# Performance work log

Hardware: AMD Instinct MI355X
Metric: run time of the kernel (lower is better)

## Reference

```python
import jax, jax.numpy as jnp
import numpy as np

N_HEAD = 16
HEAD_DIM = 128  # n_embd // n_head
RMS_EPS = 1.1920929e-07  # torch.finfo(float32).eps, F.rms_norm default
ROPE_BASE = 10000.0


def _rope_tables(T, head_dim, dtype=jnp.float32):
    half = head_dim // 2
    inv_freq = 1.0 / (ROPE_BASE ** (jnp.arange(half, dtype=jnp.float32) / half))
    t = jnp.arange(T, dtype=jnp.float32)
    freqs = jnp.outer(t, inv_freq)  # [T, half]
    return jnp.cos(freqs).astype(dtype), jnp.sin(freqs).astype(dtype)


def _apply_rope(x, cos, sin):
    # x: [B, T, H, D]; cos/sin: [T, D//2]
    half = x.shape[-1] // 2
    x1, x2 = x[..., :half], x[..., half:]
    c = cos[None, :, None, :]
    s = sin[None, :, None, :]
    return jnp.concatenate([x1 * c - x2 * s, x1 * s + x2 * c], axis=-1)


def _rms_norm(x):
    ms = jnp.mean(jnp.square(x), axis=-1, keepdims=True)
    return x * jax.lax.rsqrt(ms + RMS_EPS)


def setup_inputs() -> dict:
    key = jax.random.key(0)
    ks = jax.random.split(key, 5)
    B, T, E = 4, 2048, 2048
    x = jax.random.normal(ks[0], (B, T, E), dtype=jnp.float32)
    scale = 0.02
    wq = jax.random.normal(ks[1], (E, E), dtype=jnp.float32) * scale
    wk = jax.random.normal(ks[2], (E, E), dtype=jnp.float32) * scale
    wv = jax.random.normal(ks[3], (E, E), dtype=jnp.float32) * scale
    wo = jax.random.normal(ks[4], (E, E), dtype=jnp.float32) * scale
    return {"x": x, "wq": wq, "wk": wk, "wv": wv, "wo": wo}


def reference(x, wq, wk, wv, wo):
    B, T, E = x.shape
    H, D = N_HEAD, HEAD_DIM
    # QKV projections (bias-free linears)
    q = (x @ wq).reshape(B, T, H, D)
    k = (x @ wk).reshape(B, T, H, D)
    v = (x @ wv).reshape(B, T, H, D)
    # RoPE then parameter-free QK RMS norm
    cos, sin = _rope_tables(T, D, x.dtype)
    q = _rms_norm(_apply_rope(q, cos, sin))
    k = _rms_norm(_apply_rope(k, cos, sin))
    # causal SDPA
    scale = 1.0 / jnp.sqrt(jnp.asarray(D, dtype=x.dtype))
    scores = jnp.einsum('bqhd,bkhd->bhqk', q, k) * scale
    causal = jnp.tril(jnp.ones((T, T), dtype=bool))
    scores = jnp.where(causal[None, None], scores, jnp.asarray(-jnp.inf, scores.dtype))
    attn = jax.nn.softmax(scores, axis=-1)
    y = jnp.einsum('bhqk,bkhd->bqhd', attn, v).reshape(B, T, E)
    return y @ wo
```

## Files before the change

kernel.cpp:

```cpp
#include <hip/hip_runtime.h>
#include <math.h>

#define T_SEQ 2048
#define BATCH 4
#define E_DIM 2048
#define NHEAD 16
#define HDIM 128
#define RMS_EPS 1.1920929e-07f
#define NQT (T_SEQ / 128)

typedef unsigned short u16;
typedef __attribute__((ext_vector_type(8))) unsigned short u16x8;
typedef __attribute__((ext_vector_type(8))) short bf16x8;
typedef __attribute__((ext_vector_type(4))) float f32x4;

typedef const __attribute__((address_space(1))) unsigned int g_u32;
typedef __attribute__((address_space(3))) unsigned int l_u32;

static __device__ __forceinline__ u16 f2b(float f) {
  unsigned int u = __builtin_bit_cast(unsigned int, f);
  u += 0x7fffu + ((u >> 16) & 1u);
  return (u16)(u >> 16);
}
static __device__ __forceinline__ float b2f(u16 v) {
  return __builtin_bit_cast(float, ((unsigned int)v) << 16);
}

__global__ __launch_bounds__(256) void convert_f32_bf16(
    const float* __restrict__ src, u16* __restrict__ dst, int n) {
  int i = (blockIdx.x * 256 + threadIdx.x) * 4;
  if (i >= n) return;
  float4 v = *reinterpret_cast<const float4*>(src + i);
  ushort4 o;
  o.x = f2b(v.x); o.y = f2b(v.y); o.z = f2b(v.z); o.w = f2b(v.w);
  *reinterpret_cast<ushort4*>(dst + i) = o;
}

__global__ __launch_bounds__(256) void convt_w_k(
    const float* __restrict__ W, u16* __restrict__ Wt) {
  __shared__ u16 tile[64][72];
  int c0 = blockIdx.x * 64;
  int r0 = blockIdx.y * 64;
  int tid = threadIdx.x;
  int lrow = tid >> 2;
  int lcol = (tid & 3) * 16;
#pragma unroll
  for (int i = 0; i < 4; ++i) {
    float4 v = *reinterpret_cast<const float4*>(
        W + (long long)(r0 + lrow) * E_DIM + c0 + lcol + i * 4);
    tile[lrow][lcol + i * 4 + 0] = f2b(v.x);
    tile[lrow][lcol + i * 4 + 1] = f2b(v.y);
    tile[lrow][lcol + i * 4 + 2] = f2b(v.z);
    tile[lrow][lcol + i * 4 + 3] = f2b(v.w);
  }
  __syncthreads();
  int wrow = tid >> 2;
  int wcol = (tid & 3) * 16;
  u16 o[16];
#pragma unroll
  for (int i = 0; i < 16; ++i) o[i] = tile[wcol + i][wrow];
  u16* dst = Wt + (long long)(c0 + wrow) * E_DIM + r0 + wcol;
  *reinterpret_cast<u16x8*>(dst)     = *reinterpret_cast<u16x8*>(&o[0]);
  *reinterpret_cast<u16x8*>(dst + 8) = *reinterpret_cast<u16x8*>(&o[8]);
}

__global__ __launch_bounds__(256) void rope_tables_k(
    float* __restrict__ cost, float* __restrict__ sint) {
  int idx = blockIdx.x * 256 + threadIdx.x;
  int i = idx & 63, t = idx >> 6;
  double inv = pow(10000.0, -(double)i / 64.0);
  double ang = (double)t * inv;
  cost[idx] = (float)cos(ang);
  sint[idx] = (float)sin(ang);
}

__global__ __launch_bounds__(256) void rope_rms_k(
    u16* __restrict__ Qb, u16* __restrict__ Kb, const float* __restrict__ cost,
    const float* __restrict__ sint) {
  int half = gridDim.x >> 1;
  int isK = blockIdx.x >= half;
  u16* qk = isK ? Kb : Qb;
  float outscale = isK ? 1.0f : 0.08838834764831845f;
  int wave = threadIdx.x >> 6;
  int lane = threadIdx.x & 63;
  long long row = (long long)(blockIdx.x - (isK ? half : 0)) * 4 + wave;
  int th = (int)(row >> 4);
  int t = th & (T_SEQ - 1);
  u16* p = qk + row * HDIM;
  float x1 = b2f(p[lane]);
  float x2 = b2f(p[lane + 64]);
  float c = cost[t * 64 + lane];
  float s = sint[t * 64 + lane];
  float o1 = x1 * c - x2 * s;
  float o2 = x1 * s + x2 * c;
  float ss = o1 * o1 + o2 * o2;
#pragma unroll
  for (int m = 32; m >= 1; m >>= 1) ss += __shfl_xor(ss, m, 64);
  float r = rsqrtf(ss * (1.0f / 128.0f) + RMS_EPS) * outscale;
  p[lane] = f2b(o1 * r);
  p[lane + 64] = f2b(o2 * r);
}

__global__ __launch_bounds__(256) void transpose_v_k(
    const u16* __restrict__ V, u16* __restrict__ Vt) {
  __shared__ u16 tile[64][72];
  int t0 = blockIdx.x * 64, d0 = blockIdx.y * 64;
  int bh = blockIdx.z;
  int b = bh >> 4, h = bh & 15;
  int tid = threadIdx.x;
  int lrow = tid >> 3;
  int lcol = (tid & 7) * 8;
#pragma unroll
  for (int pass = 0; pass < 2; ++pass) {
    int row = lrow + pass * 32;
    const u16* src = V + ((((long long)b * T_SEQ + t0 + row) * NHEAD + h) << 7) + d0 + lcol;
    *reinterpret_cast<u16x8*>(&tile[row][lcol]) = *reinterpret_cast<const u16x8*>(src);
  }
  __syncthreads();
#pragma unroll
  for (int pass = 0; pass < 2; ++pass) {
    int drow = (tid >> 3) + pass * 32;
    int tcol = (tid & 7) * 8;
    u16x8 o;
#pragma unroll
    for (int i = 0; i < 8; ++i) o[i] = tile[tcol + i][drow];
    u16* dst = Vt + ((long long)bh * HDIM + d0 + drow) * T_SEQ + t0 + tcol;
    *reinterpret_cast<u16x8*>(dst) = o;
  }
}

__global__ __launch_bounds__(512, 2) void gemm_bt_k(
    const u16* __restrict__ A,
    const u16* __restrict__ Bt0, const u16* __restrict__ Bt1, const u16* __restrict__ Bt2,
    u16* __restrict__ C0, u16* __restrict__ C1, u16* __restrict__ C2,
    float* __restrict__ Cf, int M, int N, int K) {
  const u16* Bt = blockIdx.z == 0 ? Bt0 : (blockIdx.z == 1 ? Bt1 : Bt2);
  u16* C = blockIdx.z == 0 ? C0 : (blockIdx.z == 1 ? C1 : C2);
  __shared__ u16 As[2][256 * 64];
  __shared__ u16 Bs[2][256 * 64];
  const int tid = threadIdx.x;
  const int lane = tid & 63, wave = tid >> 6;
  const int wm = wave >> 2, wn = wave & 3;
  const int m0 = blockIdx.y * 256, n0 = blockIdx.x * 256;
  const int lr = lane & 15, lq = lane >> 4, l7 = lane & 7;
  const int NT = K >> 6;

  int rowA[2][2], rowB[2][2];
  const u16* gA[2][2];
  const u16* gB[2][2];
#pragma unroll
  for (int l = 0; l < 2; ++l) {
    int rihb = l * 64 + wave * 8;
#pragma unroll
    for (int h = 0; h < 2; ++h) {
      int ra = ((rihb >> 6) << 7) + h * 64 + (rihb & 63);
      int rb = ((rihb >> 5) << 6) + h * 32 + (rihb & 31);
      rowA[h][l] = ra;
      rowB[h][l] = rb;
      int rA = ra + (lane >> 3);
      int rB = rb + (lane >> 3);
      gA[h][l] = A + (long long)(m0 + rA) * K + ((l7 ^ (rA & 7)) * 8);
      gB[h][l] = Bt + (long long)(n0 + rB) * K + ((l7 ^ (rB & 7)) * 8);
    }
  }

  f32x4 acc[8][4] = {};

#define STAGE_A(tile, h)                                                      \
  do {                                                                        \
    if ((tile) < NT) {                                                        \
      int _b = (tile) & 1;                                                    \
      long long _ko = (long long)(tile) << 6;                                 \
      __builtin_amdgcn_global_load_lds((g_u32*)(gA[h][0] + _ko),              \
          (l_u32*)(&As[_b][rowA[h][0] * 64]), 16, 0, 0);                      \
      __builtin_amdgcn_global_load_lds((g_u32*)(gA[h][1] + _ko),              \
          (l_u32*)(&As[_b][rowA[h][1] * 64]), 16, 0, 0);                      \
    }                                                                         \
  } while (0)
#define STAGE_B(tile, h)                                                      \
  do {                                                                        \
    if ((tile) < NT) {                                                        \
      int _b = (tile) & 1;                                                    \
      long long _ko = (long long)(tile) << 6;                                 \
      __builtin_amdgcn_global_load_lds((g_u32*)(gB[h][0] + _ko),              \
          (l_u32*)(&Bs[_b][rowB[h][0] * 64]), 16, 0, 0);                      \
      __builtin_amdgcn_global_load_lds((g_u32*)(gB[h][1] + _ko),              \
          (l_u32*)(&Bs[_b][rowB[h][1] * 64]), 16, 0, 0);                      \
    }                                                                         \
  } while (0)

  STAGE_B(0, 0); STAGE_B(0, 1); STAGE_A(0, 0); STAGE_A(0, 1);
  STAGE_B(1, 0); STAGE_B(1, 1); STAGE_A(1, 0);
  asm volatile("s_waitcnt vmcnt(6)" ::: "memory");
  __builtin_amdgcn_s_barrier();
  __builtin_amdgcn_sched_barrier(0);

  for (int t = 0; t < NT; ++t) {
    const u16* Ab = As[t & 1];
    const u16* Bb = Bs[t & 1];
    bf16x8 aA[4][2], bB[4][2];

#define LD_A(mt, ks)                                                          \
  (*reinterpret_cast<const bf16x8*>(                                          \
      Ab + (wm * 128 + (mt) * 16 + lr) * 64 + ((((ks) << 2) + lq) ^ l7) * 8))
#define LD_B(nt, ks)                                                          \
  (*reinterpret_cast<const bf16x8*>(                                          \
      Bb + (wn * 64 + (nt) * 16 + lr) * 64 + ((((ks) << 2) + lq) ^ l7) * 8))
#define MFMA_QUAD(mh, nh)                                                     \
  _Pragma("unroll") for (int mi = 0; mi < 4; ++mi)                            \
  _Pragma("unroll") for (int ni = 0; ni < 2; ++ni)                            \
  _Pragma("unroll") for (int ks = 0; ks < 2; ++ks)                            \
    acc[(mh) * 4 + mi][(nh) * 2 + ni] =                                       \
        __builtin_amdgcn_mfma_f32_16x16x32_bf16(aA[mi][ks],                   \
            bB[(nh) * 2 + ni][ks], acc[(mh) * 4 + mi][(nh) * 2 + ni], 0, 0, 0);

#pragma unroll
    for (int mi = 0; mi < 4; ++mi) { aA[mi][0] = LD_A(mi, 0); aA[mi][1] = LD_A(mi, 1); }
#pragma unroll
    for (int ni = 0; ni < 2; ++ni) { bB[ni][0] = LD_B(ni, 0); bB[ni][1] = LD_B(ni, 1); }
    STAGE_A(t + 1, 1);
    __builtin_amdgcn_s_barrier();
    asm volatile("s_waitcnt lgkmcnt(0)" ::: "memory");
    __builtin_amdgcn_sched_barrier(0);
    __builtin_amdgcn_s_setprio(1);
    MFMA_QUAD(0, 0);
    __builtin_amdgcn_s_setprio(0);
    __builtin_amdgcn_s_barrier();

#pragma unroll
    for (int ni = 0; ni < 2; ++ni) { bB[2 + ni][0] = LD_B(2 + ni, 0); bB[2 + ni][1] = LD_B(2 + ni, 1); }
    STAGE_B(t + 2, 0);
    __builtin_amdgcn_s_barrier();
    asm volatile("s_waitcnt lgkmcnt(0)" ::: "memory");
    __builtin_amdgcn_sched_barrier(0);
    __builtin_amdgcn_s_setprio(1);
    MFMA_QUAD(0, 1);
    __builtin_amdgcn_s_setprio(0);
    __builtin_amdgcn_s_barrier();

#pragma unroll
    for (int mi = 0; mi < 4; ++mi) { aA[mi][0] = LD_A(4 + mi, 0); aA[mi][1] = LD_A(4 + mi, 1); }
    STAGE_B(t + 2, 1);
    __builtin_amdgcn_s_barrier();
    asm volatile("s_waitcnt lgkmcnt(0)" ::: "memory");
    __builtin_amdgcn_sched_barrier(0);
    __builtin_amdgcn_s_setprio(1);
    MFMA_QUAD(1, 0);
    __builtin_amdgcn_s_setprio(0);
    __builtin_amdgcn_s_barrier();

    STAGE_A(t + 2, 0);
    __builtin_amdgcn_s_barrier();
    __builtin_amdgcn_s_setprio(1);
    MFMA_QUAD(1, 1);
    __builtin_amdgcn_s_setprio(0);
    if (t < NT - 2) {
      asm volatile("s_waitcnt vmcnt(6)" ::: "memory");
    } else {
      asm volatile("s_waitcnt vmcnt(0)" ::: "memory");
    }
    __builtin_amdgcn_s_barrier();
    __builtin_amdgcn_sched_barrier(0);
  }
#undef LD_A
#undef LD_B
#undef MFMA_QUAD
#undef STAGE_A
#undef STAGE_B

#pragma unroll
  for (int mt = 0; mt < 8; ++mt)
#pragma unroll
    for (int nt = 0; nt < 4; ++nt) {
      long long col = n0 + wn * 64 + nt * 16 + lr;
#pragma unroll
      for (int r = 0; r < 4; ++r) {
        long long row = m0 + wm * 128 + mt * 16 + lq * 4 + r;
        float v = acc[mt][nt][r];
        if (Cf) Cf[row * N + col] = v;
        else C[row * N + col] = f2b(v);
      }
    }
}

__global__ __launch_bounds__(256, 3) void attn_k(
    const u16* __restrict__ Q, const u16* __restrict__ K,
    const u16* __restrict__ Vt, u16* __restrict__ Y) {
  __shared__ u16 Ks[64 * 128];
  __shared__ u16 Vs[128 * 64];
  __shared__ u16 Ps[4][32 * 72];
  __shared__ float Al[4][32];
  int pair = blockIdx.x;
  int bh = blockIdx.y;
  int b = bh >> 4, h = bh & 15;
  int tid = threadIdx.x, lane = tid & 63, wave = tid >> 6;
  int lr = lane & 15, lq = lane >> 4;

  const u16* kp[4];
  const u16* vp[4];
#pragma unroll
  for (int p = 0; p < 4; ++p) {
    int c = p * 256 + wave * 64 + lane;
    int key = c >> 4, sk = c & 15, gk = (sk - key) & 15;
    kp[p] = K + (((long long)b * T_SEQ + key) * NHEAD + h) * HDIM + gk * 8;
    int d = c >> 3, sv = c & 7, gv = (sv - d) & 7;
    vp[p] = Vt + ((long long)bh * HDIM + d) * T_SEQ + gv * 8;
  }

#pragma unroll 1
  for (int phase = 0; phase < 2; ++phase) {
    int qt = phase == 0 ? (NQT - 1 - pair) : pair;
    int qbase = qt * 128 + wave * 32;

    bf16x8 aq[2][4];
#pragma unroll
    for (int n2 = 0; n2 < 2; ++n2) {
      const u16* qp = Q + (((long long)b * T_SEQ + qbase + n2 * 16 + lr) * NHEAD + h) * HDIM;
#pragma unroll
      for (int kt = 0; kt < 4; ++kt)
        aq[n2][kt] = *reinterpret_cast<const bf16x8*>(qp + kt * 32 + lq * 8);
    }

    float m_s[2], l_s[2];
#pragma unroll
    for (int n2 = 0; n2 < 2; ++n2) { m_s[n2] = -INFINITY; l_s[n2] = 0.f; }
    f32x4 o[2][8] = {};

    int niter = 2 * qt + 2;
    for (int j = 0; j < niter; ++j) {
      __syncthreads();
#pragma unroll
      for (int p = 0; p < 4; ++p) {
        __builtin_amdgcn_global_load_lds(
            (g_u32*)(kp[p] + (long long)j * 64 * NHEAD * HDIM),
            (l_u32*)(Ks + p * 2048 + wave * 512), 16, 0, 0);
        __builtin_amdgcn_global_load_lds(
            (g_u32*)(vp[p] + j * 64),
            (l_u32*)(Vs + p * 2048 + wave * 512), 16, 0, 0);
      }
      __syncthreads();

      f32x4 s[4][2];
#pragma unroll
      for (int mt = 0; mt < 4; ++mt) {
        int key = mt * 16 + lr;
        bf16x8 ak[4];
#pragma unroll
        for (int kt = 0; kt < 4; ++kt) {
          int slot = (kt * 4 + lq + key) & 15;
          ak[kt] = *reinterpret_cast<const bf16x8*>(&Ks[key * 128 + slot * 8]);
        }
#pragma unroll
        for (int n2 = 0; n2 < 2; ++n2) {
          f32x4 acc = {};
#pragma unroll
          for (int kt = 0; kt < 4; ++kt)
            acc = __builtin_amdgcn_mfma_f32_16x16x32_bf16(ak[kt], aq[n2][kt], acc, 0, 0, 0);
          s[mt][n2] = acc;
        }
      }

      if (j >= 2 * qt) {
#pragma unroll
        for (int mt = 0; mt < 4; ++mt)
#pragma unroll
          for (int n2 = 0; n2 < 2; ++n2) {
            int q = qbase + n2 * 16 + lr;
#pragma unroll
            for (int r = 0; r < 4; ++r) {
              int key = j * 64 + mt * 16 + lq * 4 + r;
              if (key > q) s[mt][n2][r] = -INFINITY;
            }
          }
      }

      float alpha[2];
#pragma unroll
      for (int n2 = 0; n2 < 2; ++n2) {
        float mx = s[0][n2][0];
#pragma unroll
        for (int mt = 0; mt < 4; ++mt)
#pragma unroll
          for (int r = 0; r < 4; ++r) mx = fmaxf(mx, s[mt][n2][r]);
        mx = fmaxf(mx, __shfl_xor(mx, 16, 64));
        mx = fmaxf(mx, __shfl_xor(mx, 32, 64));
        float mn = fmaxf(m_s[n2], mx);
        alpha[n2] = __expf(m_s[n2] - mn);
        m_s[n2] = mn;
        float sum = 0.f;
        int q = n2 * 16 + lr;
#pragma unroll
        for (int mt = 0; mt < 4; ++mt) {
          ushort4 pk;
          float p0 = __expf(s[mt][n2][0] - mn);
          float p1 = __expf(s[mt][n2][1] - mn);
          float p2 = __expf(s[mt][n2][2] - mn);
          float p3 = __expf(s[mt][n2][3] - mn);
          sum += (p0 + p1) + (p2 + p3);
          pk.x = f2b(p0); pk.y = f2b(p1); pk.z = f2b(p2); pk.w = f2b(p3);
          *reinterpret_cast<ushort4*>(&Ps[wave][q * 72 + mt * 16 + lq * 4]) = pk;
        }
        sum += __shfl_xor(sum, 16, 64);
        sum += __shfl_xor(sum, 32, 64);
        l_s[n2] = l_s[n2] * alpha[n2] + sum;
      }

      if (lq == 0) {
        Al[wave][lr] = alpha[0];
        Al[wave][16 + lr] = alpha[1];
      }
#pragma unroll
      for (int q2 = 0; q2 < 2; ++q2) {
        f32x4 av = *reinterpret_cast<const f32x4*>(&Al[wave][q2 * 16 + lq * 4]);
#pragma unroll
        for (int r = 0; r < 4; ++r)
#pragma unroll
          for (int dt = 0; dt < 8; ++dt) o[q2][dt][r] *= av[r];
      }

#pragma unroll
      for (int kh = 0; kh < 2; ++kh) {
        bf16x8 ap[2];
#pragma unroll
        for (int q2 = 0; q2 < 2; ++q2)
          ap[q2] = *reinterpret_cast<const bf16x8*>(
              &Ps[wave][(q2 * 16 + lr) * 72 + kh * 32 + lq * 8]);
#pragma unroll
        for (int dt = 0; dt < 8; ++dt) {
          int d = dt * 16 + lr;
          int slot = (kh * 4 + lq + d) & 7;
          bf16x8 bv = *reinterpret_cast<const bf16x8*>(&Vs[d * 64 + slot * 8]);
#pragma unroll
          for (int q2 = 0; q2 < 2; ++q2)
            o[q2][dt] = __builtin_amdgcn_mfma_f32_16x16x32_bf16(ap[q2], bv, o[q2][dt], 0, 0, 0);
        }
      }
    }

    if (lq == 0) {
      Al[wave][lr] = l_s[0];
      Al[wave][16 + lr] = l_s[1];
    }
#pragma unroll
    for (int q2 = 0; q2 < 2; ++q2) {
      f32x4 lv = *reinterpret_cast<const f32x4*>(&Al[wave][q2 * 16 + lq * 4]);
#pragma unroll
      for (int r = 0; r < 4; ++r) {
        float inv = 1.0f / lv[r];
        int q = qbase + q2 * 16 + lq * 4 + r;
        u16* yp = Y + (((long long)b * T_SEQ + q) * NHEAD + h) * HDIM;
#pragma unroll
        for (int dt = 0; dt < 8; ++dt)
          yp[dt * 16 + lr] = f2b(o[q2][dt][r] * inv);
      }
    }
  }
}

extern "C" void kernel_launch(void* const* d_in, const int* in_sizes, int n_in,
                              void* d_out, int out_size, void* d_ws, size_t ws_size,
                              hipStream_t stream) {
  (void)in_sizes; (void)n_in; (void)out_size; (void)ws_size;
  const float* x  = (const float*)d_in[0];
  const float* wq = (const float*)d_in[1];
  const float* wk = (const float*)d_in[2];
  const float* wv = (const float*)d_in[3];
  const float* wo = (const float*)d_in[4];
  float* out = (float*)d_out;

  char* ws = (char*)d_ws;
  size_t off = 0;
  auto alloc = [&](size_t bytes) {
    char* p = ws + off;
    off += (bytes + 255) & ~(size_t)255;
    return p;
  };
  const size_t NTOK = (size_t)BATCH * T_SEQ;
  const size_t XE = NTOK * E_DIM;
  const size_t WE = (size_t)E_DIM * E_DIM;

  u16* xb  = (u16*)alloc(XE * 2);
  u16* wqt = (u16*)alloc(WE * 2);
  u16* wkt = (u16*)alloc(WE * 2);
  u16* wvt = (u16*)alloc(WE * 2);
  u16* wot = (u16*)alloc(WE * 2);
  u16* Qb  = (u16*)alloc(XE * 2);
  u16* Kb  = (u16*)alloc(XE * 2);
  u16* Vb  = (u16*)alloc(XE * 2);
  u16* Vt  = (u16*)alloc(XE * 2);
  u16* Yb  = (u16*)alloc(XE * 2);
  float* cost = (float*)alloc((size_t)T_SEQ * 64 * 4);
  float* sint = (float*)alloc((size_t)T_SEQ * 64 * 4);

  convert_f32_bf16<<<XE / 1024, 256, 0, stream>>>(x, xb, (int)XE);
  dim3 gw(E_DIM / 64, E_DIM / 64);
  convt_w_k<<<gw, 256, 0, stream>>>(wq, wqt);
  convt_w_k<<<gw, 256, 0, stream>>>(wk, wkt);
  convt_w_k<<<gw, 256, 0, stream>>>(wv, wvt);
  convt_w_k<<<gw, 256, 0, stream>>>(wo, wot);
  rope_tables_k<<<(T_SEQ * 64) / 256, 256, 0, stream>>>(cost, sint);

  dim3 gq(E_DIM / 256, NTOK / 256, 3);
  gemm_bt_k<<<gq, 512, 0, stream>>>(xb, wqt, wkt, wvt, Qb, Kb, Vb, nullptr,
                                    (int)NTOK, E_DIM, E_DIM);

  rope_rms_k<<<(unsigned)(NTOK * NHEAD / 4) * 2, 256, 0, stream>>>(Qb, Kb, cost, sint);

  dim3 gt(T_SEQ / 64, HDIM / 64, BATCH * NHEAD);
  transpose_v_k<<<gt, 256, 0, stream>>>(Vb, Vt);

  dim3 ga(NQT / 2, BATCH * NHEAD);
  attn_k<<<ga, 256, 0, stream>>>(Qb, Kb, Vt, Yb);

  dim3 go(E_DIM / 256, NTOK / 256, 1);
  gemm_bt_k<<<go, 512, 0, stream>>>(Yb, wot, wot, wot, nullptr, nullptr, nullptr, out,
                                    (int)NTOK, E_DIM, E_DIM);
}
```

Baseline: 685.8 us.

## Remap GEMM and attention block indices for locality and restructure GEMM MFMA phases

Remaps GEMM workgroup indices so that consecutive blocks, which the hardware distributes round-robin across XCDs, share A/B tiles within each XCD's L2. The same swizzle is applied to attention so heads land in XCD-local groups. The GEMM main loop now works on 2 M-subtiles by 4 N-subtiles per phase, which cuts A-fragment registers, and advances global pointers incrementally instead of recomputing offsets. The mapping hardcodes grid shapes, so other launch dimensions would compute wrong tiles.

```diff
diff --git a/kernel.cpp b/kernel.cpp
--- a/kernel.cpp
+++ b/kernel.cpp
@@ -134,14 +134,26 @@
     const u16* __restrict__ Bt0, const u16* __restrict__ Bt1, const u16* __restrict__ Bt2,
     u16* __restrict__ C0, u16* __restrict__ C1, u16* __restrict__ C2,
     float* __restrict__ Cf, int M, int N, int K) {
-  const u16* Bt = blockIdx.z == 0 ? Bt0 : (blockIdx.z == 1 ? Bt1 : Bt2);
-  u16* C = blockIdx.z == 0 ? C0 : (blockIdx.z == 1 ? C1 : C2);
+  int lin = blockIdx.x + (blockIdx.y << 3) + (blockIdx.z << 8);
+  int kx = lin & 7, ii = lin >> 3;
+  int by = ((kx >> 1) << 3) + (ii & 7);
+  int bx, bz;
+  if (gridDim.z == 3) {
+    int u = (kx & 1) * 12 + (ii >> 3);
+    bx = u & 7; bz = u >> 3;
+  } else {
+    bx = ((kx & 1) << 2) + (ii >> 3);
+    bz = 0;
+  }
+  const u16* Bt = bz == 0 ? Bt0 : (bz == 1 ? Bt1 : Bt2);
+  u16* C = bz == 0 ? C0 : (bz == 1 ? C1 : C2);
+
   __shared__ u16 As[2][256 * 64];
   __shared__ u16 Bs[2][256 * 64];
   const int tid = threadIdx.x;
   const int lane = tid & 63, wave = tid >> 6;
   const int wm = wave >> 2, wn = wave & 3;
-  const int m0 = blockIdx.y * 256, n0 = blockIdx.x * 256;
+  const int m0 = by * 256, n0 = bx * 256;
   const int lr = lane & 15, lq = lane >> 4, l7 = lane & 7;
   const int NT = K >> 6;
 
@@ -166,93 +178,97 @@
 
   f32x4 acc[8][4] = {};
 
-#define STAGE_A(tile, h)                                                      \
-  do {                                                                        \
-    if ((tile) < NT) {                                                        \
-      int _b = (tile) & 1;                                                    \
-      long long _ko = (long long)(tile) << 6;                                 \
-      __builtin_amdgcn_global_load_lds((g_u32*)(gA[h][0] + _ko),              \
-          (l_u32*)(&As[_b][rowA[h][0] * 64]), 16, 0, 0);                      \
-      __builtin_amdgcn_global_load_lds((g_u32*)(gA[h][1] + _ko),              \
-          (l_u32*)(&As[_b][rowA[h][1] * 64]), 16, 0, 0);                      \
-    }                                                                         \
-  } while (0)
-#define STAGE_B(tile, h)                                                      \
-  do {                                                                        \
-    if ((tile) < NT) {                                                        \
-      int _b = (tile) & 1;                                                    \
-      long long _ko = (long long)(tile) << 6;                                 \
-      __builtin_amdgcn_global_load_lds((g_u32*)(gB[h][0] + _ko),              \
-          (l_u32*)(&Bs[_b][rowB[h][0] * 64]), 16, 0, 0);                      \
-      __builtin_amdgcn_global_load_lds((g_u32*)(gB[h][1] + _ko),              \
-          (l_u32*)(&Bs[_b][rowB[h][1] * 64]), 16, 0, 0);                      \
-    }                                                                         \
-  } while (0)
-
-  STAGE_B(0, 0); STAGE_B(0, 1); STAGE_A(0, 0); STAGE_A(0, 1);
-  STAGE_B(1, 0); STAGE_B(1, 1); STAGE_A(1, 0);
-  asm volatile("s_waitcnt vmcnt(6)" ::: "memory");
-  __builtin_amdgcn_s_barrier();
-  __builtin_amdgcn_sched_barrier(0);
-
-  for (int t = 0; t < NT; ++t) {
-    const u16* Ab = As[t & 1];
-    const u16* Bb = Bs[t & 1];
-    bf16x8 aA[4][2], bB[4][2];
-
+#define GLDS(gp, lp) \
+  __builtin_amdgcn_global_load_lds((g_u32*)(gp), (l_u32*)(lp), 16, 0, 0)
 #define LD_A(mt, ks)                                                          \
   (*reinterpret_cast<const bf16x8*>(                                          \
       Ab + (wm * 128 + (mt) * 16 + lr) * 64 + ((((ks) << 2) + lq) ^ l7) * 8))
 #define LD_B(nt, ks)                                                          \
   (*reinterpret_cast<const bf16x8*>(                                          \
       Bb + (wn * 64 + (nt) * 16 + lr) * 64 + ((((ks) << 2) + lq) ^ l7) * 8))
-#define MFMA_QUAD(mh, nh)                                                     \
-  _Pragma("unroll") for (int mi = 0; mi < 4; ++mi)                            \
-  _Pragma("unroll") for (int ni = 0; ni < 2; ++ni)                            \
+#define MFMA_PH(ph)                                                           \
+  _Pragma("unroll") for (int mi = 0; mi < 2; ++mi)                            \
+  _Pragma("unroll") for (int ni = 0; ni < 4; ++ni)                            \
   _Pragma("unroll") for (int ks = 0; ks < 2; ++ks)                            \
-    acc[(mh) * 4 + mi][(nh) * 2 + ni] =                                       \
-        __builtin_amdgcn_mfma_f32_16x16x32_bf16(aA[mi][ks],                   \
-            bB[(nh) * 2 + ni][ks], acc[(mh) * 4 + mi][(nh) * 2 + ni], 0, 0, 0);
-
-#pragma unroll
-    for (int mi = 0; mi < 4; ++mi) { aA[mi][0] = LD_A(mi, 0); aA[mi][1] = LD_A(mi, 1); }
-#pragma unroll
-    for (int ni = 0; ni < 2; ++ni) { bB[ni][0] = LD_B(ni, 0); bB[ni][1] = LD_B(ni, 1); }
-    STAGE_A(t + 1, 1);
+    acc[(ph) * 2 + mi][ni] = __builtin_amdgcn_mfma_f32_16x16x32_bf16(         \
+        aA[mi][ks], bB[ni][ks], acc[(ph) * 2 + mi][ni], 0, 0, 0);
+
+  GLDS(gB[0][0], &Bs[0][rowB[0][0] * 64]); GLDS(gB[0][1], &Bs[0][rowB[0][1] * 64]);
+  GLDS(gB[1][0], &Bs[0][rowB[1][0] * 64]); GLDS(gB[1][1], &Bs[0][rowB[1][1] * 64]);
+  GLDS(gA[0][0], &As[0][rowA[0][0] * 64]); GLDS(gA[0][1], &As[0][rowA[0][1] * 64]);
+  GLDS(gA[1][0], &As[0][rowA[1][0] * 64]); GLDS(gA[1][1], &As[0][rowA[1][1] * 64]);
+  GLDS(gB[0][0] + 64, &Bs[1][rowB[0][0] * 64]); GLDS(gB[0][1] + 64, &Bs[1][rowB[0][1] * 64]);
+  GLDS(gB[1][0] + 64, &Bs[1][rowB[1][0] * 64]); GLDS(gB[1][1] + 64, &Bs[1][rowB[1][1] * 64]);
+  GLDS(gA[0][0] + 64, &As[1][rowA[0][0] * 64]); GLDS(gA[0][1] + 64, &As[1][rowA[0][1] * 64]);
+  asm volatile("s_waitcnt vmcnt(6)" ::: "memory");
+  __builtin_amdgcn_s_barrier();
+  __builtin_amdgcn_sched_barrier(0);
+
+  for (int t = 0; t < NT; ++t) {
+    const u16* Ab = As[t & 1];
+    const u16* Bb = Bs[t & 1];
+    u16* An = (u16*)As[(t & 1) ^ 1];
+    u16* Ac = (u16*)As[t & 1];
+    u16* Bc = (u16*)Bs[t & 1];
+    const bool g1 = (t + 1 < NT), g2 = (t + 2 < NT);
+    bf16x8 aA[2][2], bB[4][2];
+
+#pragma unroll
+    for (int mi = 0; mi < 2; ++mi) { aA[mi][0] = LD_A(mi, 0); aA[mi][1] = LD_A(mi, 1); }
+#pragma unroll
+    for (int ni = 0; ni < 4; ++ni) { bB[ni][0] = LD_B(ni, 0); bB[ni][1] = LD_B(ni, 1); }
+    if (g1) {
+      GLDS(gA[1][0] + 64, &An[rowA[1][0] * 64]);
+      GLDS(gA[1][1] + 64, &An[rowA[1][1] * 64]);
+    }
+    asm volatile("s_waitcnt lgkmcnt(8)" ::: "memory");
     __builtin_amdgcn_s_barrier();
     asm volatile("s_waitcnt lgkmcnt(0)" ::: "memory");
     __builtin_amdgcn_sched_barrier(0);
     __builtin_amdgcn_s_setprio(1);
-    MFMA_QUAD(0, 0);
+    MFMA_PH(0);
     __builtin_amdgcn_s_setprio(0);
     __builtin_amdgcn_s_barrier();
 
 #pragma unroll
-    for (int ni = 0; ni < 2; ++ni) { bB[2 + ni][0] = LD_B(2 + ni, 0); bB[2 + ni][1] = LD_B(2 + ni, 1); }
-    STAGE_B(t + 2, 0);
+    for (int mi = 0; mi < 2; ++mi) { aA[mi][0] = LD_A(2 + mi, 0); aA[mi][1] = LD_A(2 + mi, 1); }
+    if (g2) {
+      GLDS(gB[0][0] + 128, &Bc[rowB[0][0] * 64]);
+      GLDS(gB[0][1] + 128, &Bc[rowB[0][1] * 64]);
+    }
     __builtin_amdgcn_s_barrier();
     asm volatile("s_waitcnt lgkmcnt(0)" ::: "memory");
     __builtin_amdgcn_sched_barrier(0);
     __builtin_amdgcn_s_setprio(1);
-    MFMA_QUAD(0, 1);
+    MFMA_PH(1);
     __builtin_amdgcn_s_setprio(0);
     __builtin_amdgcn_s_barrier();
 
 #pragma unroll
-    for (int mi = 0; mi < 4; ++mi) { aA[mi][0] = LD_A(4 + mi, 0); aA[mi][1] = LD_A(4 + mi, 1); }
-    STAGE_B(t + 2, 1);
+    for (int mi = 0; mi < 2; ++mi) { aA[mi][0] = LD_A(4 + mi, 0); aA[mi][1] = LD_A(4 + mi, 1); }
+    if (g2) {
+      GLDS(gB[1][0] + 128, &Bc[rowB[1][0] * 64]);
+      GLDS(gB[1][1] + 128, &Bc[rowB[1][1] * 64]);
+    }
     __builtin_amdgcn_s_barrier();
     asm volatile("s_waitcnt lgkmcnt(0)" ::: "memory");
     __builtin_amdgcn_sched_barrier(0);
     __builtin_amdgcn_s_setprio(1);
-    MFMA_QUAD(1, 0);
+    MFMA_PH(2);
     __builtin_amdgcn_s_setprio(0);
     __builtin_amdgcn_s_barrier();
 
-    STAGE_A(t + 2, 0);
-    __builtin_amdgcn_s_barrier();
+#pragma unroll
+    for (int mi = 0; mi < 2; ++mi) { aA[mi][0] = LD_A(6 + mi, 0); aA[mi][1] = LD_A(6 + mi, 1); }
+    if (g2) {
+      GLDS(gA[0][0] + 128, &Ac[rowA[0][0] * 64]);
+      GLDS(gA[0][1] + 128, &Ac[rowA[0][1] * 64]);
+    }
+    __builtin_amdgcn_s_barrier();
+    asm volatile("s_waitcnt lgkmcnt(0)" ::: "memory");
+    __builtin_amdgcn_sched_barrier(0);
     __builtin_amdgcn_s_setprio(1);
-    MFMA_QUAD(1, 1);
+    MFMA_PH(3);
     __builtin_amdgcn_s_setprio(0);
     if (t < NT - 2) {
       asm volatile("s_waitcnt vmcnt(6)" ::: "memory");
@@ -261,12 +277,16 @@
     }
     __builtin_amdgcn_s_barrier();
     __builtin_amdgcn_sched_barrier(0);
+
+#pragma unroll
+    for (int l = 0; l < 2; ++l)
+#pragma unroll
+      for (int h = 0; h < 2; ++h) { gA[h][l] += 64; gB[h][l] += 64; }
   }
 #undef LD_A
 #undef LD_B
-#undef MFMA_QUAD
-#undef STAGE_A
-#undef STAGE_B
+#undef MFMA_PH
+#undef GLDS
 
 #pragma unroll
   for (int mt = 0; mt < 8; ++mt)
@@ -290,8 +310,9 @@
   __shared__ u16 Vs[128 * 64];
   __shared__ u16 Ps[4][32 * 72];
   __shared__ float Al[4][32];
-  int pair = blockIdx.x;
-  int bh = blockIdx.y;
+  int lin = blockIdx.x + (blockIdx.y << 3);
+  int pair = (lin >> 6);
+  int bh = ((lin & 7) << 3) + ((lin >> 3) & 7);
   int b = bh >> 4, h = bh & 15;
   int tid = threadIdx.x, lane = tid & 63, wave = tid >> 6;
   int lr = lane & 15, lq = lane >> 4;
```

New measurement: 655.7 us. 4.4% less time.
